# Performance work log

Hardware: AMD Instinct MI355X
Metric: run time of the kernel (lower is better)

Reference implementation:

```python
import jax, jax.numpy as jnp
import numpy as np


def setup_inputs() -> dict:
    key = jax.random.key(0)
    kk, kq, kv = jax.random.split(key, 3)
    B, N, S, D = 2, 16, 2048, 64
    return {
        "k": jax.random.normal(kk, (B, N, S, D), dtype=jnp.float32),
        "q": jax.random.normal(kq, (B, N, S, D), dtype=jnp.float32),
        "v": jax.random.normal(kv, (B, N, S, D), dtype=jnp.float32),
    }


def reference(k, q, v):
    # NOTE: module applies no 1/sqrt(d) scaling (inputs pre-scaled upstream).
    attn_scores = jnp.einsum("bnqd,bnkd->bnqk", q, k)  # [B, N, Sq, Sk]
    attn_probs = jax.nn.softmax(attn_scores, axis=-1)
    # dropout p=0.0 -> identity
    attn_output = jnp.einsum("bnqk,bnkd->bnqd", attn_probs, v)
    return (attn_output, attn_probs)
```

## Files before the change

### kernel.cpp

```cpp
#include <hip/hip_runtime.h>

typedef _Float16 f16;
typedef _Float16 f16x8 __attribute__((ext_vector_type(8)));
typedef float f32x4 __attribute__((ext_vector_type(4)));

#define HEADS 32
#define SEQ   2048
#define DIM   64
#define QT    64
#define KT    64
#define NT    32
#define L2E   1.44269504088896340736f

__device__ __forceinline__ void gload_lds16(const void* gsrc, void* ldst) {
  __builtin_amdgcn_global_load_lds((__attribute__((address_space(1))) void*)gsrc,
                                   (__attribute__((address_space(3))) void*)ldst, 16, 0, 0);
}

__global__ __launch_bounds__(256) void prep_kernel(const float* __restrict__ k,
                                                   const float* __restrict__ v,
                                                   char* __restrict__ kt,
                                                   f16* __restrict__ vt) {
  int n = blockIdx.x * 256 + threadIdx.x;
  const int HALF = HEADS * SEQ * (DIM / 8);
  if (n < HALF) {
    int d8 = (n & 7) * 8;
    int kv = (n >> 3) & (SEQ - 1);
    int h  = n >> 14;
    const float* src = k + ((size_t)(h * SEQ + kv)) * DIM + d8;
    float4 a = *(const float4*)src;
    float4 b = *(const float4*)(src + 4);
    f16x8 o;
    o[0]=(f16)a.x; o[1]=(f16)a.y; o[2]=(f16)a.z; o[3]=(f16)a.w;
    o[4]=(f16)b.x; o[5]=(f16)b.y; o[6]=(f16)b.z; o[7]=(f16)b.w;
    *(f16x8*)(kt + ((size_t)(h * SEQ + kv)) * 128 + ((d8 * 2) ^ ((kv & 7) << 4))) = o;
  } else {
    int m = n - HALF;
    int d   = m & 63;
    int kv8 = ((m >> 6) & 255) * 8;
    int h   = m >> 14;
    const float* src = v + ((size_t)(h * SEQ + kv8)) * DIM + d;
    f16x8 o;
#pragma unroll
    for (int i = 0; i < 8; i++) o[i] = (f16)src[i * DIM];
    *(f16x8*)(vt + ((size_t)(h * DIM + d)) * SEQ + kv8) = o;
  }
}

#define STAGE(t, buf)                                                                  \
  do {                                                                                 \
    const char* ktile_ = kthead + (size_t)(t) * KT * 128;                              \
    gload_lds16(ktile_ + tid * 16, &lds_k[buf][tid * 16]);                             \
    gload_lds16(ktile_ + 4096 + tid * 16, &lds_k[buf][4096 + tid * 16]);               \
  } while (0)

#define QKT_M(SC, buf)                                                                 \
  do {                                                                                 \
    _Pragma("unroll") for (int kc = 0; kc < 2; kc++) {                                 \
      _Pragma("unroll") for (int f = 0; f < 4; f++) {                                  \
        int row_ = f * 16 + c;                                                         \
        f16x8 kb_ = *(const f16x8*)&lds_k[buf][row_ * 128 +                            \
                       ((kc * 64 + g * 16) ^ ((row_ & 7) << 4))];                      \
        SC[f] = __builtin_amdgcn_mfma_f32_16x16x32_f16(qa[kc], kb_, SC[f], 0, 0, 0);   \
      }                                                                                \
    }                                                                                  \
  } while (0)

#define LOAD_QA                                                                        \
  do {                                                                                 \
    const float* qp = q + ((size_t)(head * SEQ + q0 + w * 16 + c)) * DIM + g * 8;      \
    _Pragma("unroll") for (int kc = 0; kc < 2; kc++) {                                 \
      float4 a = *(const float4*)(qp + kc * 32);                                       \
      float4 b = *(const float4*)(qp + kc * 32 + 4);                                   \
      qa[kc][0]=(f16)a.x; qa[kc][1]=(f16)a.y; qa[kc][2]=(f16)a.z; qa[kc][3]=(f16)a.w;  \
      qa[kc][4]=(f16)b.x; qa[kc][5]=(f16)b.y; qa[kc][6]=(f16)b.z; qa[kc][7]=(f16)b.w;  \
    }                                                                                  \
  } while (0)

__global__ __launch_bounds__(256, 8) void lsum_kernel(const float* __restrict__ q,
                                                      const char* __restrict__ kt,
                                                      float* __restrict__ rinv_out) {
  __shared__ char lds_k[2][KT * 128];

  const int tid = threadIdx.x;
  const int w = tid >> 6, l = tid & 63, g = l >> 4, c = l & 15;
  const int swz  = (blockIdx.x & 7) * 128 + (blockIdx.x >> 3);
  const int head = swz >> 5;
  const int q0   = (swz & 31) * QT;

  f16x8 qa[2];
  LOAD_QA;
  const char* kthead = kt + (size_t)head * SEQ * 128;

  float l_ln[4] = {0.f, 0.f, 0.f, 0.f};
  STAGE(0, 0);
  __syncthreads();
  for (int t = 0; t < NT; t++) {
    int cur = t & 1;
    if (t + 1 < NT) STAGE(t + 1, cur ^ 1);
    f32x4 sc[4];
#pragma unroll
    for (int f = 0; f < 4; f++) sc[f] = (f32x4){0.f, 0.f, 0.f, 0.f};
    QKT_M(sc, cur);
#pragma unroll
    for (int f = 0; f < 4; f++)
#pragma unroll
      for (int r = 0; r < 4; r++) l_ln[r] += __builtin_amdgcn_exp2f(sc[f][r] * L2E);
    __syncthreads();
  }
#pragma unroll
  for (int r = 0; r < 4; r++) {
    float lv = l_ln[r];
#pragma unroll
    for (int d = 1; d < 16; d <<= 1) lv += __shfl_xor(lv, d, 64);
    if (c == 0) rinv_out[head * SEQ + q0 + w * 16 + 4 * g + r] = 1.0f / lv;
  }
}

__global__ __launch_bounds__(256, 5) void attn_kernel(const float* __restrict__ q,
                                                      const char* __restrict__ kt,
                                                      const f16* __restrict__ vt,
                                                      const float* __restrict__ rinv_in,
                                                      float* __restrict__ out_o,
                                                      float* __restrict__ out_p) {
  __shared__ char lds_k[2][KT * 128];
  __shared__ char lds_p[QT * 128];

  const int tid = threadIdx.x;
  const int w = tid >> 6, l = tid & 63, g = l >> 4, c = l & 15;
  const int swz  = (blockIdx.x & 7) * 128 + (blockIdx.x >> 3);
  const int head = swz >> 5;
  const int q0   = (swz & 31) * QT;

  f16x8 qa[2];
  LOAD_QA;

  const char* kthead = kt + (size_t)head * SEQ * 128;
  const f16*  vhead  = vt + (size_t)head * DIM * SEQ;

  f32x4 rinv;
#pragma unroll
  for (int r = 0; r < 4; r++)
    rinv[r] = rinv_in[head * SEQ + q0 + w * 16 + 4 * g + r];

  f32x4 o_acc[4];
#pragma unroll
  for (int f = 0; f < 4; f++) o_acc[f] = (f32x4){0.f, 0.f, 0.f, 0.f};
  float* prow = out_p + (size_t)(head * SEQ + q0) * SEQ;

  STAGE(0, 0);
  __syncthreads();
  for (int t = 0; t < NT; t++) {
    int cur = t & 1;
    if (t + 1 < NT) STAGE(t + 1, cur ^ 1);

    f16x8 vb[2][4];
#pragma unroll
    for (int kc = 0; kc < 2; kc++)
#pragma unroll
      for (int f = 0; f < 4; f++)
        vb[kc][f] = *(const f16x8*)(vhead + (size_t)(f * 16 + c) * SEQ + t * 64 + kc * 32 + g * 8);

    f32x4 sc[4];
#pragma unroll
    for (int f = 0; f < 4; f++) sc[f] = (f32x4){0.f, 0.f, 0.f, 0.f};
    QKT_M(sc, cur);

#pragma unroll
    for (int f = 0; f < 4; f++)
#pragma unroll
      for (int r = 0; r < 4; r++) {
        float pv = __builtin_amdgcn_exp2f(sc[f][r] * L2E) * rinv[r];
        int rowL = w * 16 + 4 * g + r;
        __builtin_nontemporal_store(pv, &prow[(size_t)rowL * SEQ + t * 64 + f * 16 + c]);
        *(f16*)(lds_p + rowL * 128 + (((f * 16 + c) * 2) ^ ((rowL & 7) << 4))) = (f16)pv;
      }
    asm volatile("" ::: "memory");

    {
      int rowA = w * 16 + c;
#pragma unroll
      for (int kc = 0; kc < 2; kc++) {
        f16x8 pa = *(const f16x8*)(lds_p + rowA * 128 +
                                   ((kc * 64 + g * 16) ^ ((rowA & 7) << 4)));
#pragma unroll
        for (int f = 0; f < 4; f++)
          o_acc[f] = __builtin_amdgcn_mfma_f32_16x16x32_f16(pa, vb[kc][f], o_acc[f], 0, 0, 0);
      }
    }
    __syncthreads();
  }

#pragma unroll
  for (int f = 0; f < 4; f++)
#pragma unroll
    for (int r = 0; r < 4; r++)
      __builtin_nontemporal_store(o_acc[f][r],
        &out_o[(size_t)(head * SEQ + q0 + w * 16 + 4 * g + r) * DIM + f * 16 + c]);
}

extern "C" void kernel_launch(void* const* d_in, const int* in_sizes, int n_in,
                              void* d_out, int out_size, void* d_ws, size_t ws_size,
                              hipStream_t stream) {
  const float* k = (const float*)d_in[0];
  const float* q = (const float*)d_in[1];
  const float* v = (const float*)d_in[2];
  float* out_o = (float*)d_out;
  float* out_p = out_o + (size_t)HEADS * SEQ * DIM;

  char*  kt = (char*)d_ws;
  f16*   vt = (f16*)(kt + (size_t)HEADS * SEQ * DIM * 2);
  float* rs = (float*)(vt + (size_t)HEADS * SEQ * DIM);

  prep_kernel<<<dim3(4096), dim3(256), 0, stream>>>(k, v, kt, vt);
  lsum_kernel<<<dim3(1024), dim3(256), 0, stream>>>(q, kt, rs);
  attn_kernel<<<dim3(1024), dim3(256), 0, stream>>>(q, kt, vt, rs, out_o, out_p);
}
```

Measured before the change: 232.4 us.

## Swap MFMA operands so each lane owns a query row and vectorize stores

The MFMA operand order in both the QK^T and PV products is swapped, so the accumulator layout gives each lane four consecutive key (or output) columns of a single query row. This lets the probability matrix and output be written with 16-byte vector nontemporal stores instead of scalar ones, lets P go to LDS as 8-byte f16x4 writes, and cuts the row-sum reduction to two shuffles. Each lane now needs only one reciprocal row sum. The aim is to reduce store instruction count and improve coalescing on the large probability output, which dominates memory traffic. The new indexing and swizzle must match exactly to stay correct.

```diff
diff --git a/kernel.cpp b/kernel.cpp
--- a/kernel.cpp
+++ b/kernel.cpp
@@ -2,6 +2,7 @@
 
 typedef _Float16 f16;
 typedef _Float16 f16x8 __attribute__((ext_vector_type(8)));
+typedef _Float16 f16x4 __attribute__((ext_vector_type(4)));
 typedef float f32x4 __attribute__((ext_vector_type(4)));
 
 #define HEADS 32
@@ -54,14 +55,15 @@
     gload_lds16(ktile_ + 4096 + tid * 16, &lds_k[buf][4096 + tid * 16]);               \
   } while (0)
 
-#define QKT_M(SC, buf)                                                                 \
+#define QKT_S(SC, buf)                                                                 \
   do {                                                                                 \
-    _Pragma("unroll") for (int kc = 0; kc < 2; kc++) {                                 \
-      _Pragma("unroll") for (int f = 0; f < 4; f++) {                                  \
+    _Pragma("unroll") for (int f = 0; f < 4; f++) {                                    \
+      SC[f] = (f32x4){0.f, 0.f, 0.f, 0.f};                                             \
+      _Pragma("unroll") for (int kc = 0; kc < 2; kc++) {                               \
         int row_ = f * 16 + c;                                                         \
         f16x8 kb_ = *(const f16x8*)&lds_k[buf][row_ * 128 +                            \
                        ((kc * 64 + g * 16) ^ ((row_ & 7) << 4))];                      \
-        SC[f] = __builtin_amdgcn_mfma_f32_16x16x32_f16(qa[kc], kb_, SC[f], 0, 0, 0);   \
+        SC[f] = __builtin_amdgcn_mfma_f32_16x16x32_f16(kb_, qa[kc], SC[f], 0, 0, 0);   \
       }                                                                                \
     }                                                                                  \
   } while (0)
@@ -92,29 +94,23 @@
   LOAD_QA;
   const char* kthead = kt + (size_t)head * SEQ * 128;
 
-  float l_ln[4] = {0.f, 0.f, 0.f, 0.f};
+  float l_c = 0.f;
   STAGE(0, 0);
   __syncthreads();
   for (int t = 0; t < NT; t++) {
     int cur = t & 1;
     if (t + 1 < NT) STAGE(t + 1, cur ^ 1);
     f32x4 sc[4];
-#pragma unroll
-    for (int f = 0; f < 4; f++) sc[f] = (f32x4){0.f, 0.f, 0.f, 0.f};
-    QKT_M(sc, cur);
+    QKT_S(sc, cur);
 #pragma unroll
     for (int f = 0; f < 4; f++)
 #pragma unroll
-      for (int r = 0; r < 4; r++) l_ln[r] += __builtin_amdgcn_exp2f(sc[f][r] * L2E);
+      for (int r = 0; r < 4; r++) l_c += __builtin_amdgcn_exp2f(sc[f][r] * L2E);
     __syncthreads();
   }
-#pragma unroll
-  for (int r = 0; r < 4; r++) {
-    float lv = l_ln[r];
-#pragma unroll
-    for (int d = 1; d < 16; d <<= 1) lv += __shfl_xor(lv, d, 64);
-    if (c == 0) rinv_out[head * SEQ + q0 + w * 16 + 4 * g + r] = 1.0f / lv;
-  }
+  l_c += __shfl_xor(l_c, 16, 64);
+  l_c += __shfl_xor(l_c, 32, 64);
+  if (l < 16) rinv_out[head * SEQ + q0 + w * 16 + c] = 1.0f / l_c;
 }
 
 __global__ __launch_bounds__(256, 5) void attn_kernel(const float* __restrict__ q,
@@ -124,7 +120,7 @@
                                                       float* __restrict__ out_o,
                                                       float* __restrict__ out_p) {
   __shared__ char lds_k[2][KT * 128];
-  __shared__ char lds_p[QT * 128];
+  __shared__ __align__(16) char lds_p[QT * 128];
 
   const int tid = threadIdx.x;
   const int w = tid >> 6, l = tid & 63, g = l >> 4, c = l & 15;
@@ -138,15 +134,14 @@
   const char* kthead = kt + (size_t)head * SEQ * 128;
   const f16*  vhead  = vt + (size_t)head * DIM * SEQ;
 
-  f32x4 rinv;
-#pragma unroll
-  for (int r = 0; r < 4; r++)
-    rinv[r] = rinv_in[head * SEQ + q0 + w * 16 + 4 * g + r];
+  const float rinv_c = rinv_in[head * SEQ + q0 + w * 16 + c];
 
   f32x4 o_acc[4];
 #pragma unroll
   for (int f = 0; f < 4; f++) o_acc[f] = (f32x4){0.f, 0.f, 0.f, 0.f};
-  float* prow = out_p + (size_t)(head * SEQ + q0) * SEQ;
+  float* prow = out_p + (size_t)(head * SEQ + q0 + w * 16 + c) * SEQ;
+  char*  prowL = lds_p + (w * 16 + c) * 128;
+  const int swp = (c & 7) << 4;
 
   STAGE(0, 0);
   __syncthreads();
@@ -162,41 +157,35 @@
         vb[kc][f] = *(const f16x8*)(vhead + (size_t)(f * 16 + c) * SEQ + t * 64 + kc * 32 + g * 8);
 
     f32x4 sc[4];
-#pragma unroll
-    for (int f = 0; f < 4; f++) sc[f] = (f32x4){0.f, 0.f, 0.f, 0.f};
-    QKT_M(sc, cur);
-
-#pragma unroll
-    for (int f = 0; f < 4; f++)
-#pragma unroll
-      for (int r = 0; r < 4; r++) {
-        float pv = __builtin_amdgcn_exp2f(sc[f][r] * L2E) * rinv[r];
-        int rowL = w * 16 + 4 * g + r;
-        __builtin_nontemporal_store(pv, &prow[(size_t)rowL * SEQ + t * 64 + f * 16 + c]);
-        *(f16*)(lds_p + rowL * 128 + (((f * 16 + c) * 2) ^ ((rowL & 7) << 4))) = (f16)pv;
-      }
+    QKT_S(sc, cur);
+
+#pragma unroll
+    for (int f = 0; f < 4; f++) {
+#pragma unroll
+      for (int r = 0; r < 4; r++)
+        sc[f][r] = __builtin_amdgcn_exp2f(sc[f][r] * L2E) * rinv_c;
+      __builtin_nontemporal_store(sc[f], (f32x4*)&prow[t * 64 + f * 16 + 4 * g]);
+      f16x4 hv;
+#pragma unroll
+      for (int r = 0; r < 4; r++) hv[r] = (f16)sc[f][r];
+      *(f16x4*)(prowL + ((f * 32 + 8 * g) ^ swp)) = hv;
+    }
     asm volatile("" ::: "memory");
 
-    {
-      int rowA = w * 16 + c;
-#pragma unroll
-      for (int kc = 0; kc < 2; kc++) {
-        f16x8 pa = *(const f16x8*)(lds_p + rowA * 128 +
-                                   ((kc * 64 + g * 16) ^ ((rowA & 7) << 4)));
-#pragma unroll
-        for (int f = 0; f < 4; f++)
-          o_acc[f] = __builtin_amdgcn_mfma_f32_16x16x32_f16(pa, vb[kc][f], o_acc[f], 0, 0, 0);
-      }
+#pragma unroll
+    for (int kc = 0; kc < 2; kc++) {
+      f16x8 pa = *(const f16x8*)(prowL + ((kc * 64 + g * 16) ^ swp));
+#pragma unroll
+      for (int f = 0; f < 4; f++)
+        o_acc[f] = __builtin_amdgcn_mfma_f32_16x16x32_f16(vb[kc][f], pa, o_acc[f], 0, 0, 0);
     }
     __syncthreads();
   }
 
 #pragma unroll
   for (int f = 0; f < 4; f++)
-#pragma unroll
-    for (int r = 0; r < 4; r++)
-      __builtin_nontemporal_store(o_acc[f][r],
-        &out_o[(size_t)(head * SEQ + q0 + w * 16 + 4 * g + r) * DIM + f * 16 + c]);
+    __builtin_nontemporal_store(o_acc[f],
+      (f32x4*)&out_o[(size_t)(head * SEQ + q0 + w * 16 + c) * DIM + f * 16 + 4 * g]);
 }
 
 extern "C" void kernel_launch(void* const* d_in, const int* in_sizes, int n_in,
```

Result: faster. 206.9 us (-11.0%).
